# Optimization experiments

Hardware: AMD Instinct MI355X
Metric: run time of the kernel (lower is better)

The kernel has to match this reference:

```python
import jax, jax.numpy as jnp
import numpy as np

B, T, C = 8, 2048, 1024   # batch, seq_len, n_embd
HS = 1024                 # head_size


def setup_inputs() -> dict:
    key = jax.random.key(0)
    k1, k2, k3, k4 = jax.random.split(key, 4)
    x = jax.random.normal(k1, (B, T, C), dtype=jnp.float32)
    k_wei = jax.random.normal(k2, (C, HS), dtype=jnp.float32) * (C ** -0.5)
    q_wei = jax.random.normal(k3, (C, HS), dtype=jnp.float32) * (C ** -0.5)
    v_wei = jax.random.normal(k4, (C, HS), dtype=jnp.float32) * (C ** -0.5)
    mask = jnp.tril(jnp.ones((T, T), dtype=bool))  # causal tril, block_size >= T
    return {"x": x, "k_wei": k_wei, "q_wei": q_wei, "v_wei": v_wei, "mask": mask}


def reference(x, k_wei, q_wei, v_wei, mask):
    Bb, Tt, Cc = x.shape
    k = x @ k_wei                                   # [B,T,HS]
    q = x @ q_wei                                   # [B,T,HS]
    v = x @ v_wei                                   # [B,T,HS]
    # NOTE: source scales by C**-0.5 where C = n_embd (input channels)
    wei = jnp.einsum('bqh,bkh->bqk', q, k) * (Cc ** -0.5)  # [B,T,T]
    wei = jnp.where(mask[:Tt, :Tt], wei, -jnp.inf)
    wei = jax.nn.softmax(wei, axis=-1)
    out = wei @ v                                   # [B,T,HS]
    return out
```

## Files before the change

kernel.cpp:

```cpp
#include <hip/hip_runtime.h>
#include <hip/hip_bf16.h>
#include <stdint.h>

typedef __attribute__((ext_vector_type(4))) float f32x4;
typedef __attribute__((ext_vector_type(8))) short s16x8;

#define BARRIER() asm volatile("s_barrier" ::: "memory")
#define WAITV4()  asm volatile("s_waitcnt vmcnt(4)" ::: "memory")
#define WAITV0()  asm volatile("s_waitcnt vmcnt(0)" ::: "memory")
#define MFMA(a, b, c) __builtin_amdgcn_mfma_f32_16x16x32_bf16((a), (b), (c), 0, 0, 0)

__device__ __forceinline__ ushort f2bf(float f) {
  union { float f; uint32_t u; } v; v.f = f;
  uint32_t r = v.u + 0x7FFFu + ((v.u >> 16) & 1u);
  return (ushort)(r >> 16);
}

__device__ __forceinline__ void gload_lds16(const ushort* g, short* l) {
  __builtin_amdgcn_global_load_lds(
      (const __attribute__((address_space(1))) uint32_t*)g,
      (__attribute__((address_space(3))) uint32_t*)l, 16, 0, 0);
}

__device__ __forceinline__ int xcd_swz(int flat, int q) {
  return (flat & 7) * q + (flat >> 3);
}

__device__ __forceinline__ void stage128(const ushort* __restrict__ g, int ld,
                                         int row0, int k0, short* lbase, int tid) {
  const int w  = tid >> 6;
  const int l  = tid & 63;
  const int lr = l >> 3;
  const int ls = l & 7;
  const ushort* gp = g + (size_t)(row0 + lr) * ld + k0 + ((ls ^ lr) << 3);
  short* lp = lbase + l * 8;
#pragma unroll
  for (int i = 0; i < 4; ++i) {
    const int R0 = w * 32 + i * 8;
    gload_lds16(gp + (size_t)R0 * ld, lp + R0 * 64);
  }
}

__device__ __forceinline__ void gemm_core(
    const ushort* __restrict__ A, int lda, const ushort* __restrict__ Bt, int ldb,
    int m0, int n0, int nk, short* lds, f32x4 acc[4][4])
{
  const int tid  = threadIdx.x;
  const int lane = tid & 63, wid = tid >> 6;
  const int wr = wid >> 1, wc = wid & 1;
  const int fr = lane & 15, kg = lane >> 4;
  const int s0  = (kg ^ (fr & 7)) << 3;
  const int aro = (wr * 64 + fr) * 64;
  const int bro = (wc * 64 + fr) * 64;

  short* Ab0 = lds;            short* Bb0 = lds + 8192;
  short* Ab1 = lds + 16384;    short* Bb1 = lds + 24576;

#pragma unroll
  for (int i = 0; i < 4; ++i)
#pragma unroll
    for (int j = 0; j < 4; ++j)
      acc[i][j] = (f32x4){0.f, 0.f, 0.f, 0.f};

  stage128(A, lda, m0, 0, Ab0, tid);
  stage128(Bt, ldb, n0, 0, Bb0, tid);
  if (nk > 1) stage128(Bt, ldb, n0, 64, Bb1, tid);

#pragma unroll 1
  for (int X = 0; X < nk; ++X) {
    const int cur = X & 1;
    short* Ac = cur ? Ab1 : Ab0;
    short* Bc = cur ? Bb1 : Bb0;
    short* An = cur ? Ab0 : Ab1;

    if (X + 1 < nk) { WAITV4(); } else { WAITV0(); }
    BARRIER();
    if (X + 1 < nk) stage128(A, lda, m0, (X + 1) * 64, An, tid);

    s16x8 b[4][2], a[2][2];
#pragma unroll
    for (int ni = 0; ni < 4; ++ni) {
      b[ni][0] = *(const s16x8*)(Bc + bro + ni * 1024 + s0);
      b[ni][1] = *(const s16x8*)(Bc + bro + ni * 1024 + (s0 ^ 32));
    }
#pragma unroll
    for (int mi = 0; mi < 2; ++mi) {
      a[mi][0] = *(const s16x8*)(Ac + aro + mi * 1024 + s0);
      a[mi][1] = *(const s16x8*)(Ac + aro + mi * 1024 + (s0 ^ 32));
    }
    __builtin_amdgcn_s_setprio(1);
#pragma unroll
    for (int mi = 0; mi < 2; ++mi)
#pragma unroll
      for (int ni = 0; ni < 4; ++ni) {
        acc[mi][ni] = MFMA(a[mi][0], b[ni][0], acc[mi][ni]);
        acc[mi][ni] = MFMA(a[mi][1], b[ni][1], acc[mi][ni]);
      }
    __builtin_amdgcn_s_setprio(0);

    BARRIER();
    if (X + 2 < nk) stage128(Bt, ldb, n0, (X + 2) * 64, Bc, tid);
#pragma unroll
    for (int mi = 0; mi < 2; ++mi) {
      a[mi][0] = *(const s16x8*)(Ac + aro + (2 + mi) * 1024 + s0);
      a[mi][1] = *(const s16x8*)(Ac + aro + (2 + mi) * 1024 + (s0 ^ 32));
    }
    __builtin_amdgcn_s_setprio(1);
#pragma unroll
    for (int mi = 0; mi < 2; ++mi)
#pragma unroll
      for (int ni = 0; ni < 4; ++ni) {
        acc[2 + mi][ni] = MFMA(a[mi][0], b[ni][0], acc[2 + mi][ni]);
        acc[2 + mi][ni] = MFMA(a[mi][1], b[ni][1], acc[2 + mi][ni]);
      }
    __builtin_amdgcn_s_setprio(0);
  }
}

__global__ void cvt_x(const float* __restrict__ x, ushort* __restrict__ xb)
{
  const size_t i = (size_t)(blockIdx.x * 256 + threadIdx.x) * 4;
  const f32x4 t = *(const f32x4*)(x + i);
  uint2 pk;
  pk.x = (uint32_t)f2bf(t[0]) | ((uint32_t)f2bf(t[1]) << 16);
  pk.y = (uint32_t)f2bf(t[2]) | ((uint32_t)f2bf(t[3]) << 16);
  *(uint2*)(xb + i) = pk;
}

__global__ void cvt_w(const float* __restrict__ kw, const float* __restrict__ qw,
                      const float* __restrict__ vw, ushort* __restrict__ wt)
{
  __shared__ float t[32][33];
  const float* w = (blockIdx.z == 0) ? qw : (blockIdx.z == 1) ? kw : vw;
  const int n0 = blockIdx.x * 32, k0 = blockIdx.y * 32;
  t[threadIdx.y][threadIdx.x] = w[(size_t)(k0 + threadIdx.y) * 1024 + n0 + threadIdx.x];
  __syncthreads();
  wt[(size_t)blockIdx.z * 1048576 + (size_t)(n0 + threadIdx.y) * 1024 + k0 + threadIdx.x] =
      f2bf(t[threadIdx.x][threadIdx.y]);
}

__global__ __launch_bounds__(256) void gemm_qkv_impl(
    const ushort* __restrict__ xb, const ushort* __restrict__ wt,
    ushort* __restrict__ q, ushort* __restrict__ k, ushort* __restrict__ vT)
{
  extern __shared__ short lds[];
  const int nf = xcd_swz(blockIdx.x + 24 * blockIdx.y, 384);
  const int n0 = (nf % 24) * 128;
  const int m0 = (nf / 24) * 128;
  f32x4 acc[4][4];
  gemm_core(xb, 1024, wt, 1024, m0, n0, 16, lds, acc);

  const int lane = threadIdx.x & 63;
  const int wid = threadIdx.x >> 6;
  const int wr = wid >> 1, wc = wid & 1;
  const int q4 = (lane >> 4) << 2;
  const int fr = lane & 15;
  const int z  = n0 >> 10;
  const int cb = (n0 & 1023) + wc * 64 + fr;
  ushort* o = (z == 0) ? q : k;
#pragma unroll
  for (int mi = 0; mi < 4; ++mi)
#pragma unroll
    for (int ni = 0; ni < 4; ++ni)
#pragma unroll
      for (int j = 0; j < 4; ++j) {
        const int r = m0 + wr * 64 + mi * 16 + q4 + j;
        const int c = cb + ni * 16;
        const ushort hv = f2bf(acc[mi][ni][j]);
        if (z < 2) o[(size_t)r * 1024 + c] = hv;
        else       vT[((size_t)(r >> 11) * 1024 + c) * 2048 + (r & 2047)] = hv;
      }
}

__global__ __launch_bounds__(256) void gemm_sp(
    const ushort* __restrict__ q, const ushort* __restrict__ k,
    ushort* __restrict__ P, float* __restrict__ sums)
{
  extern __shared__ short lds[];
  float* rowsum = (float*)(lds + 32768);
  const int nf = xcd_swz(blockIdx.x + 16 * (blockIdx.y + 16 * blockIdx.z), 256);
  const int kt = nf & 15, qt = (nf >> 4) & 15, b = nf >> 8;
  if (kt > qt) return;
  f32x4 acc[4][4];
  const ushort* qb = q + (size_t)b * (2048 * 1024);
  const ushort* kb = k + (size_t)b * (2048 * 1024);
  gemm_core(qb, 1024, kb, 1024, qt * 128, kt * 128, 16, lds, acc);

  const int tid  = threadIdx.x;
  const int lane = tid & 63, wid = tid >> 6;
  const int wr = wid >> 1, wc = wid & 1;
  const int q4 = (lane >> 4) << 2;
  const int fr = lane & 15;
  const int diag = (kt == qt);
  ushort* Pb = P + ((size_t)b << 22);

#pragma unroll
  for (int mi = 0; mi < 4; ++mi)
#pragma unroll
    for (int j = 0; j < 4; ++j) {
      const int rloc = wr * 64 + mi * 16 + q4 + j;
      const int rg   = qt * 128 + rloc;
      float s = 0.f;
#pragma unroll
      for (int ni = 0; ni < 4; ++ni) {
        const int cg = kt * 128 + wc * 64 + ni * 16 + fr;
        float e = __expf(acc[mi][ni][j] * 0.03125f - 10.f);
        if (diag && cg > rg) e = 0.f;
        s += e;
        Pb[(size_t)rg * 2048 + cg] = f2bf(e);
      }
#pragma unroll
      for (int m = 1; m < 16; m <<= 1) s += __shfl_xor(s, m);
      if (fr == 0) rowsum[wc * 128 + rloc] = s;
    }
  __syncthreads();
  if (tid < 128) {
    const float tot = rowsum[tid] + rowsum[128 + tid];
    atomicAdd(&sums[b * 2048 + qt * 128 + tid], tot);
  }
}

__global__ __launch_bounds__(256) void gemm_pv(
    const ushort* __restrict__ P, const ushort* __restrict__ vT,
    const float* __restrict__ sums, float* __restrict__ out)
{
  extern __shared__ short lds[];
  const int nf = xcd_swz(blockIdx.x + 8 * (blockIdx.y + 16 * blockIdx.z), 128);
  const int ht = nf & 7, qt = (nf >> 3) & 15, b = nf >> 7;
  f32x4 acc[4][4];
  const ushort* Pb = P  + ((size_t)b << 22);
  const ushort* Vb = vT + (size_t)b * (1024 * 2048);
  gemm_core(Pb, 2048, Vb, 2048, qt * 128, ht * 128, (qt + 1) * 2, lds, acc);

  float* ob = out + (size_t)b * 2097152;
  const int lane = threadIdx.x & 63;
  const int wid = threadIdx.x >> 6;
  const int wr = wid >> 1, wc = wid & 1;
  const int r0 = qt * 128 + wr * 64 + ((lane >> 4) << 2);
  const int c0 = ht * 128 + wc * 64 + (lane & 15);
#pragma unroll
  for (int mi = 0; mi < 4; ++mi)
#pragma unroll
    for (int j = 0; j < 4; ++j) {
      const int r = r0 + mi * 16 + j;
      const float inv = 1.0f / sums[b * 2048 + r];
#pragma unroll
      for (int ni = 0; ni < 4; ++ni)
        ob[(size_t)r * 1024 + (c0 + ni * 16)] = acc[mi][ni][j] * inv;
    }
}

extern "C" void kernel_launch(void* const* d_in, const int* in_sizes, int n_in,
                              void* d_out, int out_size, void* d_ws, size_t ws_size,
                              hipStream_t stream)
{
  const float* x  = (const float*)d_in[0];
  const float* kw = (const float*)d_in[1];
  const float* qw = (const float*)d_in[2];
  const float* vw = (const float*)d_in[3];
  float* out = (float*)d_out;
  char* ws = (char*)d_ws;

  ushort* xb   = (ushort*)ws;
  ushort* P    = (ushort*)ws;
  float*  sums = (float*)(ws + 67108864);
  ushort* wt   = (ushort*)(ws + 67174400);
  ushort* q    = (ushort*)(ws + 73465856);
  ushort* k    = (ushort*)(ws + 107020288);
  ushort* vT   = (ushort*)(ws + 140574720);

  const int LDSB  = 65536;
  const int LDSB2 = 65536 + 1024;
  hipFuncSetAttribute((const void*)gemm_qkv_impl, hipFuncAttributeMaxDynamicSharedMemorySize, LDSB);
  hipFuncSetAttribute((const void*)gemm_sp,       hipFuncAttributeMaxDynamicSharedMemorySize, LDSB2);
  hipFuncSetAttribute((const void*)gemm_pv,       hipFuncAttributeMaxDynamicSharedMemorySize, LDSB);

  hipMemsetAsync(sums, 0, 8 * 2048 * sizeof(float), stream);
  cvt_x<<<16384, 256, 0, stream>>>(x, xb);
  cvt_w<<<dim3(32, 32, 3), dim3(32, 32), 0, stream>>>(kw, qw, vw, wt);
  gemm_qkv_impl<<<dim3(24, 128), 256, LDSB, stream>>>(xb, wt, q, k, vT);
  gemm_sp<<<dim3(16, 16, 8), 256, LDSB2, stream>>>(q, k, P, sums);
  gemm_pv<<<dim3(8, 16, 8), 256, LDSB, stream>>>(P, vT, sums, out);
}
```

Before: 286.0 us.

## Triple-buffer A tiles in GEMM core and remap QKV blocks per XCD

The shared GEMM core now keeps three LDS buffers for the A operand and two for B, so the A tile is prefetched two iterations ahead instead of one. The wait count rises from vmcnt(4) to vmcnt(8) to match the deeper set of loads in flight. The QKV GEMM also assigns each XCD a contiguous 64x6 block of output tiles, which should improve L2 reuse of x and weight tiles. LDS per block grows to 80KB for all three GEMMs, which may lower occupancy, and gemm_sp now reuses the staging buffer for its row-sum scratch after a sync.

```diff
diff --git a/kernel.cpp b/kernel.cpp
--- a/kernel.cpp
+++ b/kernel.cpp
@@ -6,7 +6,7 @@
 typedef __attribute__((ext_vector_type(8))) short s16x8;
 
 #define BARRIER() asm volatile("s_barrier" ::: "memory")
-#define WAITV4()  asm volatile("s_waitcnt vmcnt(4)" ::: "memory")
+#define WAITV8()  asm volatile("s_waitcnt vmcnt(8)" ::: "memory")
 #define WAITV0()  asm volatile("s_waitcnt vmcnt(0)" ::: "memory")
 #define MFMA(a, b, c) __builtin_amdgcn_mfma_f32_16x16x32_bf16((a), (b), (c), 0, 0, 0)
 
@@ -53,8 +53,11 @@
   const int aro = (wr * 64 + fr) * 64;
   const int bro = (wc * 64 + fr) * 64;
 
-  short* Ab0 = lds;            short* Bb0 = lds + 8192;
-  short* Ab1 = lds + 16384;    short* Bb1 = lds + 24576;
+  short* Ar  = lds;
+  short* An1 = lds + 8192;
+  short* An2 = lds + 16384;
+  short* Br  = lds + 24576;
+  short* Bn  = lds + 32768;
 
 #pragma unroll
   for (int i = 0; i < 4; ++i)
@@ -62,31 +65,29 @@
     for (int j = 0; j < 4; ++j)
       acc[i][j] = (f32x4){0.f, 0.f, 0.f, 0.f};
 
-  stage128(A, lda, m0, 0, Ab0, tid);
-  stage128(Bt, ldb, n0, 0, Bb0, tid);
-  if (nk > 1) stage128(Bt, ldb, n0, 64, Bb1, tid);
+  stage128(A, lda, m0, 0, Ar, tid);
+  stage128(Bt, ldb, n0, 0, Br, tid);
+  if (nk > 1) {
+    stage128(A, lda, m0, 64, An1, tid);
+    stage128(Bt, ldb, n0, 64, Bn, tid);
+  }
 
 #pragma unroll 1
   for (int X = 0; X < nk; ++X) {
-    const int cur = X & 1;
-    short* Ac = cur ? Ab1 : Ab0;
-    short* Bc = cur ? Bb1 : Bb0;
-    short* An = cur ? Ab0 : Ab1;
-
-    if (X + 1 < nk) { WAITV4(); } else { WAITV0(); }
+    if (X + 1 < nk) { WAITV8(); } else { WAITV0(); }
     BARRIER();
-    if (X + 1 < nk) stage128(A, lda, m0, (X + 1) * 64, An, tid);
+    if (X + 2 < nk) stage128(A, lda, m0, (X + 2) * 64, An2, tid);
 
     s16x8 b[4][2], a[2][2];
 #pragma unroll
     for (int ni = 0; ni < 4; ++ni) {
-      b[ni][0] = *(const s16x8*)(Bc + bro + ni * 1024 + s0);
-      b[ni][1] = *(const s16x8*)(Bc + bro + ni * 1024 + (s0 ^ 32));
+      b[ni][0] = *(const s16x8*)(Br + bro + ni * 1024 + s0);
+      b[ni][1] = *(const s16x8*)(Br + bro + ni * 1024 + (s0 ^ 32));
     }
 #pragma unroll
     for (int mi = 0; mi < 2; ++mi) {
-      a[mi][0] = *(const s16x8*)(Ac + aro + mi * 1024 + s0);
-      a[mi][1] = *(const s16x8*)(Ac + aro + mi * 1024 + (s0 ^ 32));
+      a[mi][0] = *(const s16x8*)(Ar + aro + mi * 1024 + s0);
+      a[mi][1] = *(const s16x8*)(Ar + aro + mi * 1024 + (s0 ^ 32));
     }
     __builtin_amdgcn_s_setprio(1);
 #pragma unroll
@@ -99,11 +100,11 @@
     __builtin_amdgcn_s_setprio(0);
 
     BARRIER();
-    if (X + 2 < nk) stage128(Bt, ldb, n0, (X + 2) * 64, Bc, tid);
+    if (X + 2 < nk) stage128(Bt, ldb, n0, (X + 2) * 64, Br, tid);
 #pragma unroll
     for (int mi = 0; mi < 2; ++mi) {
-      a[mi][0] = *(const s16x8*)(Ac + aro + (2 + mi) * 1024 + s0);
-      a[mi][1] = *(const s16x8*)(Ac + aro + (2 + mi) * 1024 + (s0 ^ 32));
+      a[mi][0] = *(const s16x8*)(Ar + aro + (2 + mi) * 1024 + s0);
+      a[mi][1] = *(const s16x8*)(Ar + aro + (2 + mi) * 1024 + (s0 ^ 32));
     }
     __builtin_amdgcn_s_setprio(1);
 #pragma unroll
@@ -114,6 +115,9 @@
         acc[2 + mi][ni] = MFMA(a[mi][1], b[ni][1], acc[2 + mi][ni]);
       }
     __builtin_amdgcn_s_setprio(0);
+
+    short* t = Ar; Ar = An1; An1 = An2; An2 = t;
+    t = Br; Br = Bn; Bn = t;
   }
 }
 
@@ -144,9 +148,11 @@
     ushort* __restrict__ q, ushort* __restrict__ k, ushort* __restrict__ vT)
 {
   extern __shared__ short lds[];
-  const int nf = xcd_swz(blockIdx.x + 24 * blockIdx.y, 384);
-  const int n0 = (nf % 24) * 128;
-  const int m0 = (nf / 24) * 128;
+  const int flat = blockIdx.x + 24 * blockIdx.y;
+  const int xcd = flat & 7, c = flat >> 3;
+  const int mloc = c / 6, nloc = c - mloc * 6;
+  const int m0 = ((xcd & 1) * 64 + mloc) * 128;
+  const int n0 = ((xcd >> 1) * 6 + nloc) * 128;
   f32x4 acc[4][4];
   gemm_core(xb, 1024, wt, 1024, m0, n0, 16, lds, acc);
 
@@ -165,10 +171,10 @@
 #pragma unroll
       for (int j = 0; j < 4; ++j) {
         const int r = m0 + wr * 64 + mi * 16 + q4 + j;
-        const int c = cb + ni * 16;
+        const int c2 = cb + ni * 16;
         const ushort hv = f2bf(acc[mi][ni][j]);
-        if (z < 2) o[(size_t)r * 1024 + c] = hv;
-        else       vT[((size_t)(r >> 11) * 1024 + c) * 2048 + (r & 2047)] = hv;
+        if (z < 2) o[(size_t)r * 1024 + c2] = hv;
+        else       vT[((size_t)(r >> 11) * 1024 + c2) * 2048 + (r & 2047)] = hv;
       }
 }
 
@@ -177,7 +183,6 @@
     ushort* __restrict__ P, float* __restrict__ sums)
 {
   extern __shared__ short lds[];
-  float* rowsum = (float*)(lds + 32768);
   const int nf = xcd_swz(blockIdx.x + 16 * (blockIdx.y + 16 * blockIdx.z), 256);
   const int kt = nf & 15, qt = (nf >> 4) & 15, b = nf >> 8;
   if (kt > qt) return;
@@ -185,6 +190,8 @@
   const ushort* qb = q + (size_t)b * (2048 * 1024);
   const ushort* kb = k + (size_t)b * (2048 * 1024);
   gemm_core(qb, 1024, kb, 1024, qt * 128, kt * 128, 16, lds, acc);
+  __syncthreads();
+  float* rowsum = (float*)lds;
 
   const int tid  = threadIdx.x;
   const int lane = tid & 63, wid = tid >> 6;
@@ -269,16 +276,15 @@
   ushort* k    = (ushort*)(ws + 107020288);
   ushort* vT   = (ushort*)(ws + 140574720);
 
-  const int LDSB  = 65536;
-  const int LDSB2 = 65536 + 1024;
+  const int LDSB = 81920;
   hipFuncSetAttribute((const void*)gemm_qkv_impl, hipFuncAttributeMaxDynamicSharedMemorySize, LDSB);
-  hipFuncSetAttribute((const void*)gemm_sp,       hipFuncAttributeMaxDynamicSharedMemorySize, LDSB2);
+  hipFuncSetAttribute((const void*)gemm_sp,       hipFuncAttributeMaxDynamicSharedMemorySize, LDSB);
   hipFuncSetAttribute((const void*)gemm_pv,       hipFuncAttributeMaxDynamicSharedMemorySize, LDSB);
 
   hipMemsetAsync(sums, 0, 8 * 2048 * sizeof(float), stream);
   cvt_x<<<16384, 256, 0, stream>>>(x, xb);
   cvt_w<<<dim3(32, 32, 3), dim3(32, 32), 0, stream>>>(kw, qw, vw, wt);
   gemm_qkv_impl<<<dim3(24, 128), 256, LDSB, stream>>>(xb, wt, q, k, vT);
-  gemm_sp<<<dim3(16, 16, 8), 256, LDSB2, stream>>>(q, k, P, sums);
+  gemm_sp<<<dim3(16, 16, 8), 256, LDSB, stream>>>(q, k, P, sums);
   gemm_pv<<<dim3(8, 16, 8), 256, LDSB, stream>>>(P, vT, sums, out);
 }
```

Result: slower. 315.4 us (+10.3%).

## Stage V transpose through LDS, remap QKV tiles per XCD, shrink score-kernel LDS

Applied to the files above, without the earlier changes.

The QKV GEMM epilogue for the V part now writes the 128x128 tile transposed into LDS and then emits contiguous 16-byte vector stores to vT, replacing strided 2-byte scattered stores. Block-to-tile mapping changes to a custom per-XCD grouping (each XCD covers a 64-row by 6-column-tile region) to improve L2 reuse of X and W. The score kernel reuses the GEMM LDS buffer for row sums after a barrier, so dynamic LDS drops to 64KB, which may allow higher occupancy. The added barriers and the LDS round-trip add some epilogue cost.

```diff
diff --git a/kernel.cpp b/kernel.cpp
--- a/kernel.cpp
+++ b/kernel.cpp
@@ -144,32 +144,57 @@
     ushort* __restrict__ q, ushort* __restrict__ k, ushort* __restrict__ vT)
 {
   extern __shared__ short lds[];
-  const int nf = xcd_swz(blockIdx.x + 24 * blockIdx.y, 384);
-  const int n0 = (nf % 24) * 128;
-  const int m0 = (nf / 24) * 128;
+  const int flat = blockIdx.x + 24 * blockIdx.y;
+  const int xcd = flat & 7, c = flat >> 3;
+  const int mloc = c / 6, nloc = c - mloc * 6;
+  const int m0 = ((xcd & 1) * 64 + mloc) * 128;
+  const int n0 = ((xcd >> 1) * 6 + nloc) * 128;
   f32x4 acc[4][4];
   gemm_core(xb, 1024, wt, 1024, m0, n0, 16, lds, acc);
 
-  const int lane = threadIdx.x & 63;
-  const int wid = threadIdx.x >> 6;
+  const int tid  = threadIdx.x;
+  const int lane = tid & 63;
+  const int wid  = tid >> 6;
   const int wr = wid >> 1, wc = wid & 1;
   const int q4 = (lane >> 4) << 2;
   const int fr = lane & 15;
   const int z  = n0 >> 10;
-  const int cb = (n0 & 1023) + wc * 64 + fr;
-  ushort* o = (z == 0) ? q : k;
-#pragma unroll
-  for (int mi = 0; mi < 4; ++mi)
-#pragma unroll
-    for (int ni = 0; ni < 4; ++ni)
-#pragma unroll
-      for (int j = 0; j < 4; ++j) {
-        const int r = m0 + wr * 64 + mi * 16 + q4 + j;
-        const int c = cb + ni * 16;
-        const ushort hv = f2bf(acc[mi][ni][j]);
-        if (z < 2) o[(size_t)r * 1024 + c] = hv;
-        else       vT[((size_t)(r >> 11) * 1024 + c) * 2048 + (r & 2047)] = hv;
-      }
+
+  if (z < 2) {
+    ushort* o = (z == 0) ? q : k;
+    const int cb = (n0 & 1023) + wc * 64 + fr;
+#pragma unroll
+    for (int mi = 0; mi < 4; ++mi)
+#pragma unroll
+      for (int ni = 0; ni < 4; ++ni)
+#pragma unroll
+        for (int j = 0; j < 4; ++j) {
+          const int r = m0 + wr * 64 + mi * 16 + q4 + j;
+          o[(size_t)r * 1024 + cb + ni * 16] = f2bf(acc[mi][ni][j]);
+        }
+  } else {
+    __syncthreads();
+    ushort* tr = (ushort*)lds;
+#pragma unroll
+    for (int mi = 0; mi < 4; ++mi)
+#pragma unroll
+      for (int ni = 0; ni < 4; ++ni)
+#pragma unroll
+        for (int j = 0; j < 4; ++j) {
+          const int cl = wc * 64 + ni * 16 + fr;
+          const int rl = wr * 64 + mi * 16 + q4 + j;
+          tr[cl * 136 + rl] = f2bf(acc[mi][ni][j]);
+        }
+    __syncthreads();
+    const int cl   = tid >> 1;
+    const int half = tid & 1;
+    const ushort* src = tr + cl * 136 + half * 64;
+    ushort* dst = vT + ((size_t)(m0 >> 11) * 1024 + (n0 & 1023) + cl) * 2048
+                     + (m0 & 2047) + half * 64;
+#pragma unroll
+    for (int i = 0; i < 8; ++i)
+      *(s16x8*)(dst + i * 8) = *(const s16x8*)(src + i * 8);
+  }
 }
 
 __global__ __launch_bounds__(256) void gemm_sp(
@@ -177,7 +202,6 @@
     ushort* __restrict__ P, float* __restrict__ sums)
 {
   extern __shared__ short lds[];
-  float* rowsum = (float*)(lds + 32768);
   const int nf = xcd_swz(blockIdx.x + 16 * (blockIdx.y + 16 * blockIdx.z), 256);
   const int kt = nf & 15, qt = (nf >> 4) & 15, b = nf >> 8;
   if (kt > qt) return;
@@ -185,6 +209,8 @@
   const ushort* qb = q + (size_t)b * (2048 * 1024);
   const ushort* kb = k + (size_t)b * (2048 * 1024);
   gemm_core(qb, 1024, kb, 1024, qt * 128, kt * 128, 16, lds, acc);
+  __syncthreads();
+  float* rowsum = (float*)lds;
 
   const int tid  = threadIdx.x;
   const int lane = tid & 63, wid = tid >> 6;
@@ -269,16 +295,15 @@
   ushort* k    = (ushort*)(ws + 107020288);
   ushort* vT   = (ushort*)(ws + 140574720);
 
-  const int LDSB  = 65536;
-  const int LDSB2 = 65536 + 1024;
+  const int LDSB = 65536;
   hipFuncSetAttribute((const void*)gemm_qkv_impl, hipFuncAttributeMaxDynamicSharedMemorySize, LDSB);
-  hipFuncSetAttribute((const void*)gemm_sp,       hipFuncAttributeMaxDynamicSharedMemorySize, LDSB2);
+  hipFuncSetAttribute((const void*)gemm_sp,       hipFuncAttributeMaxDynamicSharedMemorySize, LDSB);
   hipFuncSetAttribute((const void*)gemm_pv,       hipFuncAttributeMaxDynamicSharedMemorySize, LDSB);
 
   hipMemsetAsync(sums, 0, 8 * 2048 * sizeof(float), stream);
   cvt_x<<<16384, 256, 0, stream>>>(x, xb);
   cvt_w<<<dim3(32, 32, 3), dim3(32, 32), 0, stream>>>(kw, qw, vw, wt);
   gemm_qkv_impl<<<dim3(24, 128), 256, LDSB, stream>>>(xb, wt, q, k, vT);
-  gemm_sp<<<dim3(16, 16, 8), 256, LDSB2, stream>>>(q, k, P, sums);
+  gemm_sp<<<dim3(16, 16, 8), 256, LDSB, stream>>>(q, k, P, sums);
   gemm_pv<<<dim3(8, 16, 8), 256, LDSB, stream>>>(P, vT, sums, out);
 }
```

Measured after the change: 258.4 us. -9.6%, faster.
